# Optimization experiments

Measured on AMD Instinct MI355X. Metric: run time of the kernel, lower is better.

## Reference

```python
import jax, jax.numpy as jnp
import numpy as np

HEADS = 16
THETA = 10000.0


def _rope(x, pos):
    # x: [b, h, s, d_k], pos: [b, s] int
    d_k = x.shape[-1]
    inv_freq = 1.0 / (THETA ** (jnp.arange(0, d_k, 2, dtype=jnp.float32) / d_k))  # [d_k/2]
    ang = pos[..., None].astype(jnp.float32) * inv_freq                           # [b, s, d_k/2]
    cos = jnp.cos(ang)[:, None, :, :]  # [b, 1, s, d_k/2] broadcast over heads
    sin = jnp.sin(ang)[:, None, :, :]
    x_even = x[..., 0::2]
    x_odd = x[..., 1::2]
    r_even = x_even * cos - x_odd * sin
    r_odd = x_even * sin + x_odd * cos
    return jnp.stack([r_even, r_odd], axis=-1).reshape(x.shape)


def setup_inputs() -> dict:
    key = jax.random.key(0)
    ks = jax.random.split(key, 5)
    B, S, D = 4, 2048, 1024
    std = float(np.sqrt(1.0 / D))
    def w(k):
        return jnp.clip(jax.random.normal(k, (D, D), jnp.float32) * std, -3 * std, 3 * std)
    return {
        "x": jax.random.normal(ks[0], (B, S, D), jnp.float32),
        "token_positions": jnp.broadcast_to(jnp.arange(S, dtype=jnp.int32), (B, S)),
        "wq": w(ks[1]),
        "wk": w(ks[2]),
        "wv": w(ks[3]),
        "wo": w(ks[4]),
    }


def reference(x, token_positions, wq, wk, wv, wo):
    B, S, D = x.shape
    h = HEADS
    dk = D // h
    # Projections: einsum 'hd d, ... s d -> ... s hd' == x @ W.T
    def proj(w):
        return jnp.einsum('bsd,kd->bsk', x, w).reshape(B, S, h, dk).transpose(0, 2, 1, 3)
    q = _rope(proj(wq), token_positions)  # [b,h,s,dk]
    k = _rope(proj(wk), token_positions)
    v = proj(wv)
    scores = jnp.einsum('bhqd,bhkd->bhqk', q, k) / np.sqrt(dk).astype(np.float32)
    causal = jnp.tril(jnp.ones((S, S), bool))
    scores = jnp.where(causal, scores, jnp.finfo(scores.dtype).min)
    attn = jax.nn.softmax(scores, axis=-1)
    out = jnp.einsum('bhqk,bhkd->bhqd', attn, v)        # [b,h,s,dk]
    out = out.transpose(0, 2, 1, 3).reshape(B, S, D)    # [b,s,h*dk]
    return jnp.einsum('bsv,dv->bsd', out, wo)
```

## Files before the change

### kernel.cpp

```cpp
#include <hip/hip_runtime.h>
#include <hip/hip_bf16.h>
#include <stdint.h>

typedef __bf16 bf16;
typedef __bf16 bf16x4 __attribute__((ext_vector_type(4)));
typedef __bf16 bf16x8 __attribute__((ext_vector_type(8)));
typedef float f32x4 __attribute__((ext_vector_type(4)));
typedef float f32x16 __attribute__((ext_vector_type(16)));

#define GLDS16(g, l) __builtin_amdgcn_global_load_lds( \
    (const __attribute__((address_space(1))) void*)(g), \
    (__attribute__((address_space(3))) void*)(l), 16, 0, 0)

static constexpr int S = 2048;

__global__ __launch_bounds__(256) void cvt_all(const float* __restrict__ x,
                                               const float* __restrict__ wq,
                                               const float* __restrict__ wk,
                                               const float* __restrict__ wv,
                                               const float* __restrict__ wo,
                                               const int* __restrict__ tp,
                                               bf16* __restrict__ xb,
                                               bf16* __restrict__ wqkvb,
                                               bf16* __restrict__ wob,
                                               bf16* __restrict__ tabc,
                                               bf16* __restrict__ tabs) {
  const int bid = blockIdx.x;
  if (bid >= 6144) {
    int idx = (bid - 6144) * 256 + threadIdx.x;
    int row = idx >> 5, pp = idx & 31;
    float p = (float)tp[row];
    float ang = p * exp2f((float)pp * -0.4152410118609203f);
    float sn, cs;
    sincosf(ang, &sn, &cs);
    tabc[idx] = (bf16)cs;
    tabs[idx] = (bf16)sn;
    return;
  }
  const float* src;
  bf16* dst;
  int i;
  if (bid < 4096) {
    src = x; dst = xb; i = bid * 256 + threadIdx.x;
  } else {
    int w = (bid - 4096) >> 9;
    i = ((bid - 4096) & 511) * 256 + threadIdx.x;
    src = (w == 0) ? wq : (w == 1) ? wk : (w == 2) ? wv : wo;
    dst = (w == 3) ? wob : wqkvb + (size_t)w * 1048576;
  }
  const float4* p = (const float4*)src + (size_t)i * 2;
  float4 a = p[0], b = p[1];
  bf16x8 o;
  o[0] = (bf16)a.x; o[1] = (bf16)a.y; o[2] = (bf16)a.z; o[3] = (bf16)a.w;
  o[4] = (bf16)b.x; o[5] = (bf16)b.y; o[6] = (bf16)b.z; o[7] = (bf16)b.w;
  *((bf16x8*)dst + i) = o;
}

template <int MODE>
__global__ __launch_bounds__(256, 3) void gemm_k(const bf16* __restrict__ xA,
                                                 const bf16* __restrict__ wB,
                                                 const bf16* __restrict__ tabc,
                                                 const bf16* __restrict__ tabs,
                                                 bf16* __restrict__ oq,
                                                 bf16* __restrict__ ok,
                                                 bf16* __restrict__ ov,
                                                 float* __restrict__ outf) {
  constexpr int K = 1024;
  __shared__ __align__(16) char lds[49152];
  const int t = threadIdx.x, l = t & 63, wid = t >> 6;
  const int wm = wid >> 1, wn = wid & 1;
  const int bm = blockIdx.x, bn = blockIdx.y;

  int sel, tA, tB;
  const bf16 *Ap, *Bp;
  if (MODE == 0) {
    if (bn < 16) {
      sel = bn >> 3;
      tA = bm;
      tB = bn & 7;
      Ap = xA + (size_t)tA * 128 * K;
      Bp = wB + (size_t)(sel * 1024 + tB * 128) * K;
    } else {
      sel = 2;
      tA = bn - 16;
      tB = bm;
      Ap = wB + (size_t)(2048 + tA * 128) * K;
      Bp = xA + (size_t)tB * 128 * K;
    }
  } else {
    sel = 3;
    tA = bm; tB = bn;
    Ap = xA + (size_t)tA * 128 * K;
    Bp = wB + (size_t)tB * 128 * K;
  }

  const int lrow = l >> 2;
  const int csrc = ((l & 3) ^ ((l >> 3) & 3)) * 8;
  const bf16* aS = Ap + (size_t)(wid * 32 + lrow) * K + csrc;
  const bf16* bS = Bp + (size_t)(wid * 32 + lrow) * K + csrc;

  auto stage = [&](int kt, char* base) {
    GLDS16(aS + kt, base + (wid * 32) * 64);
    GLDS16(aS + (size_t)16 * K + kt, base + (wid * 32 + 16) * 64);
    GLDS16(bS + kt, base + 8192 + (wid * 32) * 64);
    GLDS16(bS + (size_t)16 * K + kt, base + 8192 + (wid * 32 + 16) * 64);
  };

  int offA[4], offB[4];
#pragma unroll
  for (int f = 0; f < 4; f++) {
    int ra = wm * 64 + f * 16 + (l & 15);
    offA[f] = ra * 64 + (((l >> 4) ^ ((ra >> 1) & 3)) * 16);
    int rb = wn * 64 + f * 16 + (l & 15);
    offB[f] = 8192 + rb * 64 + (((l >> 4) ^ ((rb >> 1) & 3)) * 16);
  }

  f32x4 acc[4][4] = {};

  char* cur = lds;
  char* nxt = lds + 16384;
  char* ovr = lds + 32768;
  stage(0, cur);
  stage(32, nxt);
#pragma unroll 1
  for (int t_ = 0; t_ < 32; ++t_) {
    if (t_ + 2 < 32) {
      stage((t_ + 2) * 32, ovr);
      asm volatile("s_waitcnt vmcnt(8)" ::: "memory");
    } else if (t_ + 1 < 32) {
      asm volatile("s_waitcnt vmcnt(4)" ::: "memory");
    } else {
      asm volatile("s_waitcnt vmcnt(0)" ::: "memory");
    }
    __builtin_amdgcn_s_barrier();
    __builtin_amdgcn_sched_barrier(0);

    bf16x8 af[4], bg[4];
#pragma unroll
    for (int f = 0; f < 4; f++) {
      af[f] = *(const bf16x8*)(cur + offA[f]);
      bg[f] = *(const bf16x8*)(cur + offB[f]);
    }
    __builtin_amdgcn_s_setprio(1);
#pragma unroll
    for (int mi = 0; mi < 4; mi++)
#pragma unroll
      for (int ni = 0; ni < 4; ni++)
        acc[mi][ni] = __builtin_amdgcn_mfma_f32_16x16x32_bf16(
            af[mi], bg[ni], acc[mi][ni], 0, 0, 0);
    __builtin_amdgcn_s_setprio(0);
    asm volatile("s_waitcnt lgkmcnt(0)" ::: "memory");
    __builtin_amdgcn_sched_barrier(0);
    __builtin_amdgcn_s_barrier();
    char* tmp = cur; cur = nxt; nxt = ovr; ovr = tmp;
  }

  if (MODE == 2) {
    const int rbase = tA * 128 + wm * 64 + (l >> 4) * 4;
    const int cbase = tB * 128 + wn * 64 + (l & 15);
#pragma unroll
    for (int mi = 0; mi < 4; mi++)
#pragma unroll
      for (int ni = 0; ni < 4; ni++)
#pragma unroll
        for (int r = 0; r < 4; r++)
          outf[(size_t)(rbase + mi * 16 + r) * 1024 + cbase + ni * 16] =
              acc[mi][ni][r];
    return;
  }

#pragma unroll
  for (int mi = 0; mi < 4; mi++)
#pragma unroll
    for (int ni = 0; ni < 4; ni++)
#pragma unroll
      for (int r = 0; r < 4; r++) {
        int row = wm * 64 + mi * 16 + (l >> 4) * 4 + r;
        int col = wn * 64 + ni * 16 + (l & 15);
        *(bf16*)(lds + row * 272 + col * 2) = (bf16)acc[mi][ni][r];
      }
  __syncthreads();

#pragma unroll 2
  for (int i = 0; i < 8; ++i) {
    const int id = t + 256 * i;
    const int row = id >> 4, ch = id & 15;
    bf16x8 v8 = *(const bf16x8*)(lds + row * 272 + ch * 16);
    if (sel < 2) {
      const int m = tA * 128 + row;
      const int g = ch & 7;
      bf16x4 tc = *(const bf16x4*)(tabc + m * 32 + g * 4);
      bf16x4 tsn = *(const bf16x4*)(tabs + m * 32 + g * 4);
      bf16x8 o;
#pragma unroll
      for (int j = 0; j < 4; j++) {
        float cs = (float)tc[j], sn = (float)tsn[j];
        float e = (float)v8[2 * j], od = (float)v8[2 * j + 1];
        o[2 * j]     = (bf16)(e * cs - od * sn);
        o[2 * j + 1] = (bf16)(e * sn + od * cs);
      }
      bf16* dst = (sel == 0) ? oq : ok;
      const int h = tB * 2 + (ch >> 3);
      size_t idx = ((size_t)((m >> 11) * 16 + h) << 17) +
                   ((size_t)(m & 2047) << 6) + g * 8;
      *(bf16x8*)(dst + idx) = o;
    } else {
      const int dd = tA * 128 + row;
      const int h = dd >> 6;
      const int s0 = tB * 128 + ch * 8;
      size_t idx = ((size_t)((s0 >> 11) * 16 + h) << 17) +
                   ((size_t)(dd & 63) << 11) + (s0 & 2047);
      *(bf16x8*)(ov + idx) = v8;
    }
  }
}

__global__ __launch_bounds__(512, 4) void attn_k(const bf16* __restrict__ q,
                                                 const bf16* __restrict__ k,
                                                 const bf16* __restrict__ vt,
                                                 bf16* __restrict__ att) {
  __shared__ bf16 Ks[3][4096];
  __shared__ bf16 Vs[3][4096];

  const int t = threadIdx.x, l = t & 63, w = t >> 6;
  const int hi2 = l >> 5, q5 = l & 31;

  const int raw = blockIdx.x;
  const int r2 = raw & 255;
  const int wg = (r2 & 7) * 32 + (r2 >> 3);
  const int bh = ((raw < 256) ? 0 : 32) + (wg >> 3);
  const int qt = (raw < 256) ? (wg & 7) : 7 - (wg & 7);

  const bf16* qb = q + (size_t)bh * S * 64;
  const bf16* kb = k + (size_t)bh * S * 64;
  const bf16* vb = vt + (size_t)bh * 64 * S;

  const int lrow = l >> 3;
  const int clog = ((l & 7) ^ (lrow & 7)) * 8;

  auto stage = [&](int nt, int b) {
    GLDS16(kb + (size_t)(nt * 64 + w * 8 + lrow) * 64 + clog, &Ks[b][w * 512]);
    GLDS16(vb + (size_t)(w * 8 + lrow) * S + nt * 64 + clog, &Vs[b][w * 512]);
  };

  const int swz = (q5 & 7) << 4;
  int kaddr[4], vaddr[8];
#pragma unroll
  for (int c = 0; c < 4; c++)
    kaddr[c] = q5 * 128 + ((32 * c + 16 * hi2) ^ swz);
#pragma unroll
  for (int m = 0; m < 8; m++)
    vaddr[m] = q5 * 128 + ((16 * m) ^ swz) + 8 * hi2;

  const int b_ = bh >> 4, h_ = bh & 15;
  const char* KsB = (const char*)&Ks[0][0];
  const char* VsB = (const char*)&Vs[0][0];

  const int wqbase = qt * 256 + w * 32;
  const int qrow = wqbase + q5;
  bf16x8 qf[4];
#pragma unroll
  for (int c = 0; c < 4; c++) {
    bf16x8 rq = *(const bf16x8*)&qb[(size_t)qrow * 64 + 16 * c + 8 * hi2];
    bf16x8 s_;
#pragma unroll
    for (int j2 = 0; j2 < 8; j2++)
      s_[j2] = (bf16)((float)rq[j2] * 0.18033688011112042f);
    qf[c] = s_;
  }

  f32x16 acc[2] = {};
  float l_r = 0.f;
  const int nkv = 4 * qt + 4;
  const int qmaxw = wqbase + 31;

  int cur = 0, nxt = 1, ovr = 2;
  stage(0, 0);
  stage(1, 1);
#pragma unroll 1
  for (int nt = 0; nt < nkv; ++nt) {
    if (nt + 2 < nkv) {
      stage(nt + 2, ovr);
      asm volatile("s_waitcnt vmcnt(4)" ::: "memory");
    } else if (nt + 1 < nkv) {
      asm volatile("s_waitcnt vmcnt(2)" ::: "memory");
    } else {
      asm volatile("s_waitcnt vmcnt(0)" ::: "memory");
    }
    __builtin_amdgcn_s_barrier();
    __builtin_amdgcn_sched_barrier(0);

    const bool live = (64 * nt) <= qmaxw;
    if (live) {
      const int bo = cur * 8192;
      float rs = 0.f;
#pragma unroll
      for (int T = 0; T < 2; T++) {
        f32x16 sc = {};
        __builtin_amdgcn_s_setprio(1);
#pragma unroll
        for (int c = 0; c < 4; c++) {
          bf16x8 kf = *(const bf16x8*)(KsB + bo + T * 4096 + kaddr[c]);
          sc = __builtin_amdgcn_mfma_f32_32x32x16_bf16(kf, qf[c], sc, 0, 0, 0);
        }
        __builtin_amdgcn_s_setprio(0);

        if (64 * nt + 32 * T + 31 > wqbase) {
#pragma unroll
          for (int r = 0; r < 16; r++) {
            int kvg = 64 * nt + 32 * T + (r & 3) + 8 * (r >> 2) + 4 * hi2;
            if (kvg > qrow) sc[r] = -1e30f;
          }
        }

        bf16x8 pa0, pa1;
#pragma unroll
        for (int r = 0; r < 8; r++) {
          float p0 = __builtin_amdgcn_exp2f(sc[r]);
          float p1 = __builtin_amdgcn_exp2f(sc[8 + r]);
          rs += p0 + p1;
          pa0[r] = (bf16)p0;
          pa1[r] = (bf16)p1;
        }

        __builtin_amdgcn_s_setprio(1);
#pragma unroll
        for (int dt = 0; dt < 2; dt++) {
          bf16x4 v0 = *(const bf16x4*)(VsB + bo + dt * 4096 + vaddr[4 * T]);
          bf16x4 v1 = *(const bf16x4*)(VsB + bo + dt * 4096 + vaddr[4 * T + 1]);
          bf16x8 bv;
#pragma unroll
          for (int j2 = 0; j2 < 4; j2++) { bv[j2] = v0[j2]; bv[4 + j2] = v1[j2]; }
          acc[dt] = __builtin_amdgcn_mfma_f32_32x32x16_bf16(pa0, bv, acc[dt], 0, 0, 0);
          v0 = *(const bf16x4*)(VsB + bo + dt * 4096 + vaddr[4 * T + 2]);
          v1 = *(const bf16x4*)(VsB + bo + dt * 4096 + vaddr[4 * T + 3]);
#pragma unroll
          for (int j2 = 0; j2 < 4; j2++) { bv[j2] = v0[j2]; bv[4 + j2] = v1[j2]; }
          acc[dt] = __builtin_amdgcn_mfma_f32_32x32x16_bf16(pa1, bv, acc[dt], 0, 0, 0);
        }
        __builtin_amdgcn_s_setprio(0);
      }
      rs += __shfl_xor(rs, 32);
      l_r += rs;
    }

    asm volatile("s_waitcnt lgkmcnt(0)" ::: "memory");
    __builtin_amdgcn_sched_barrier(0);
    __builtin_amdgcn_s_barrier();
    int t3 = cur; cur = nxt; nxt = ovr; ovr = t3;
  }

  float linv = 1.f / l_r;
#pragma unroll
  for (int r = 0; r < 16; r++) {
    int rmap = (r & 3) + 8 * (r >> 2) + 4 * hi2;
    float li = __shfl(linv, rmap);
    int rowq = wqbase + rmap;
    size_t rb = ((size_t)(b_ * S + rowq) << 10) + h_ * 64 + q5;
#pragma unroll
    for (int dt = 0; dt < 2; dt++)
      att[rb + 32 * dt] = (bf16)(acc[dt][r] * li);
  }
}

extern "C" void kernel_launch(void* const* d_in, const int* in_sizes, int n_in,
                              void* d_out, int out_size, void* d_ws, size_t ws_size,
                              hipStream_t stream) {
  const float* x  = (const float*)d_in[0];
  const int* tp   = (const int*)d_in[1];
  const float* wq = (const float*)d_in[2];
  const float* wk = (const float*)d_in[3];
  const float* wv = (const float*)d_in[4];
  const float* wo = (const float*)d_in[5];
  float* out = (float*)d_out;

  char* ws = (char*)d_ws;
  const size_t TEN = 16777216;
  bf16* x_bf    = (bf16*)(ws);
  bf16* q_bf    = (bf16*)(ws + TEN);
  bf16* k_bf    = (bf16*)(ws + 2 * TEN);
  bf16* v_bf    = (bf16*)(ws + 3 * TEN);
  bf16* wqkv_bf = (bf16*)(ws + 4 * TEN);
  bf16* wo_bf   = wqkv_bf + 3 * 1048576;
  bf16* tabc    = wo_bf + 1048576;
  bf16* tabs    = tabc + 262144;
  bf16* att_bf  = x_bf;

  cvt_all<<<7168, 256, 0, stream>>>(x, wq, wk, wv, wo, tp, x_bf, wqkv_bf,
                                    wo_bf, tabc, tabs);

  dim3 gq(64, 24);
  gemm_k<0><<<gq, 256, 0, stream>>>(x_bf, wqkv_bf, tabc, tabs, q_bf, k_bf,
                                    v_bf, nullptr);

  attn_k<<<512, 512, 0, stream>>>(q_bf, k_bf, v_bf, att_bf);

  dim3 go(64, 8);
  gemm_k<2><<<go, 256, 0, stream>>>(att_bf, wo_bf, nullptr, nullptr, nullptr,
                                    nullptr, nullptr, out);
}
```

Before: 154.4 us.

## Use 32x32x16 MFMA with two-wave 128-thread GEMM blocks

Reworks the projection and output GEMM kernel to run 2 waves per 128x128 tile instead of 4. Each wave now computes a 128x64 subtile with 32x32x16 bf16 MFMAs in place of 16x16x32. Global-to-LDS staging, the LDS swizzle, the wait counts and the epilogue index mapping are all rewritten to match. The aim is fewer LDS fragment reads per MFMA and higher per-wave arithmetic intensity, at the cost of more accumulator registers per wave and fewer waves to hide latency.

```diff
diff --git a/kernel.cpp b/kernel.cpp
--- a/kernel.cpp
+++ b/kernel.cpp
@@ -57,7 +57,7 @@
 }
 
 template <int MODE>
-__global__ __launch_bounds__(256, 3) void gemm_k(const bf16* __restrict__ xA,
+__global__ __launch_bounds__(128, 2) void gemm_k(const bf16* __restrict__ xA,
                                                  const bf16* __restrict__ wB,
                                                  const bf16* __restrict__ tabc,
                                                  const bf16* __restrict__ tabs,
@@ -67,9 +67,9 @@
                                                  float* __restrict__ outf) {
   constexpr int K = 1024;
   __shared__ __align__(16) char lds[49152];
-  const int t = threadIdx.x, l = t & 63, wid = t >> 6;
-  const int wm = wid >> 1, wn = wid & 1;
+  const int t = threadIdx.x, l = t & 63, w = t >> 6;
   const int bm = blockIdx.x, bn = blockIdx.y;
+  const int l5 = l & 31, hi = l >> 5;
 
   int sel, tA, tB;
   const bf16 *Ap, *Bp;
@@ -95,27 +95,41 @@
   }
 
   const int lrow = l >> 2;
-  const int csrc = ((l & 3) ^ ((l >> 3) & 3)) * 8;
-  const bf16* aS = Ap + (size_t)(wid * 32 + lrow) * K + csrc;
-  const bf16* bS = Bp + (size_t)(wid * 32 + lrow) * K + csrc;
+  const int swe = (((l >> 3) & 3) ^ ((l >> 5) & 1));
+  const int cs_e = ((l & 3) ^ swe) * 8;
+  const int cs_o = ((l & 3) ^ swe ^ 2) * 8;
+  const bf16* aS = Ap + (size_t)(w * 64 + lrow) * K;
+  const bf16* bS = Bp + (size_t)(w * 64 + lrow) * K;
 
   auto stage = [&](int kt, char* base) {
-    GLDS16(aS + kt, base + (wid * 32) * 64);
-    GLDS16(aS + (size_t)16 * K + kt, base + (wid * 32 + 16) * 64);
-    GLDS16(bS + kt, base + 8192 + (wid * 32) * 64);
-    GLDS16(bS + (size_t)16 * K + kt, base + 8192 + (wid * 32 + 16) * 64);
+#pragma unroll
+    for (int g = 0; g < 4; g++) {
+      const int cs = (g & 1) ? cs_o : cs_e;
+      GLDS16(aS + (size_t)(g * 16) * K + kt + cs, base + (w * 64 + g * 16) * 64);
+      GLDS16(bS + (size_t)(g * 16) * K + kt + cs,
+             base + 8192 + (w * 64 + g * 16) * 64);
+    }
   };
 
-  int offA[4], offB[4];
-#pragma unroll
-  for (int f = 0; f < 4; f++) {
-    int ra = wm * 64 + f * 16 + (l & 15);
-    offA[f] = ra * 64 + (((l >> 4) ^ ((ra >> 1) & 3)) * 16);
-    int rb = wn * 64 + f * 16 + (l & 15);
-    offB[f] = 8192 + rb * 64 + (((l >> 4) ^ ((rb >> 1) & 3)) * 16);
-  }
-
-  f32x4 acc[4][4] = {};
+  int offA[4][2], offB[2][2];
+#pragma unroll
+  for (int mi = 0; mi < 4; mi++)
+#pragma unroll
+    for (int kc = 0; kc < 2; kc++) {
+      int ra = mi * 32 + l5;
+      int swr = ((ra >> 1) ^ (ra >> 3)) & 3;
+      offA[mi][kc] = ra * 64 + (((2 * kc + hi) ^ swr) * 16);
+    }
+#pragma unroll
+  for (int ni = 0; ni < 2; ni++)
+#pragma unroll
+    for (int kc = 0; kc < 2; kc++) {
+      int rb = w * 64 + ni * 32 + l5;
+      int swr = ((rb >> 1) ^ (rb >> 3)) & 3;
+      offB[ni][kc] = 8192 + rb * 64 + (((2 * kc + hi) ^ swr) * 16);
+    }
+
+  f32x16 acc[4][2] = {};
 
   char* cur = lds;
   char* nxt = lds + 16384;
@@ -126,28 +140,36 @@
   for (int t_ = 0; t_ < 32; ++t_) {
     if (t_ + 2 < 32) {
       stage((t_ + 2) * 32, ovr);
+      asm volatile("s_waitcnt vmcnt(16)" ::: "memory");
+    } else if (t_ + 1 < 32) {
       asm volatile("s_waitcnt vmcnt(8)" ::: "memory");
-    } else if (t_ + 1 < 32) {
-      asm volatile("s_waitcnt vmcnt(4)" ::: "memory");
     } else {
       asm volatile("s_waitcnt vmcnt(0)" ::: "memory");
     }
     __builtin_amdgcn_s_barrier();
     __builtin_amdgcn_sched_barrier(0);
 
-    bf16x8 af[4], bg[4];
-#pragma unroll
-    for (int f = 0; f < 4; f++) {
-      af[f] = *(const bf16x8*)(cur + offA[f]);
-      bg[f] = *(const bf16x8*)(cur + offB[f]);
-    }
+    bf16x8 af[4][2], bg[2][2];
+#pragma unroll
+    for (int mi = 0; mi < 4; mi++)
+#pragma unroll
+      for (int kc = 0; kc < 2; kc++)
+        af[mi][kc] = *(const bf16x8*)(cur + offA[mi][kc]);
+#pragma unroll
+    for (int ni = 0; ni < 2; ni++)
+#pragma unroll
+      for (int kc = 0; kc < 2; kc++)
+        bg[ni][kc] = *(const bf16x8*)(cur + offB[ni][kc]);
+
     __builtin_amdgcn_s_setprio(1);
 #pragma unroll
     for (int mi = 0; mi < 4; mi++)
 #pragma unroll
-      for (int ni = 0; ni < 4; ni++)
-        acc[mi][ni] = __builtin_amdgcn_mfma_f32_16x16x32_bf16(
-            af[mi], bg[ni], acc[mi][ni], 0, 0, 0);
+      for (int ni = 0; ni < 2; ni++)
+#pragma unroll
+        for (int kc = 0; kc < 2; kc++)
+          acc[mi][ni] = __builtin_amdgcn_mfma_f32_32x32x16_bf16(
+              af[mi][kc], bg[ni][kc], acc[mi][ni], 0, 0, 0);
     __builtin_amdgcn_s_setprio(0);
     asm volatile("s_waitcnt lgkmcnt(0)" ::: "memory");
     __builtin_amdgcn_sched_barrier(0);
@@ -156,34 +178,34 @@
   }
 
   if (MODE == 2) {
-    const int rbase = tA * 128 + wm * 64 + (l >> 4) * 4;
-    const int cbase = tB * 128 + wn * 64 + (l & 15);
 #pragma unroll
     for (int mi = 0; mi < 4; mi++)
 #pragma unroll
-      for (int ni = 0; ni < 4; ni++)
-#pragma unroll
-        for (int r = 0; r < 4; r++)
-          outf[(size_t)(rbase + mi * 16 + r) * 1024 + cbase + ni * 16] =
-              acc[mi][ni][r];
+      for (int ni = 0; ni < 2; ni++)
+#pragma unroll
+        for (int r = 0; r < 16; r++) {
+          int gm = tA * 128 + mi * 32 + (r & 3) + 8 * (r >> 2) + 4 * hi;
+          int gn = tB * 128 + w * 64 + ni * 32 + l5;
+          outf[(size_t)gm * 1024 + gn] = acc[mi][ni][r];
+        }
     return;
   }
 
 #pragma unroll
   for (int mi = 0; mi < 4; mi++)
 #pragma unroll
-    for (int ni = 0; ni < 4; ni++)
-#pragma unroll
-      for (int r = 0; r < 4; r++) {
-        int row = wm * 64 + mi * 16 + (l >> 4) * 4 + r;
-        int col = wn * 64 + ni * 16 + (l & 15);
+    for (int ni = 0; ni < 2; ni++)
+#pragma unroll
+      for (int r = 0; r < 16; r++) {
+        int row = mi * 32 + (r & 3) + 8 * (r >> 2) + 4 * hi;
+        int col = w * 64 + ni * 32 + l5;
         *(bf16*)(lds + row * 272 + col * 2) = (bf16)acc[mi][ni][r];
       }
   __syncthreads();
 
 #pragma unroll 2
-  for (int i = 0; i < 8; ++i) {
-    const int id = t + 256 * i;
+  for (int i = 0; i < 16; ++i) {
+    const int id = t + 128 * i;
     const int row = id >> 4, ch = id & 15;
     bf16x8 v8 = *(const bf16x8*)(lds + row * 272 + ch * 16);
     if (sel < 2) {
@@ -390,12 +412,12 @@
                                     wo_bf, tabc, tabs);
 
   dim3 gq(64, 24);
-  gemm_k<0><<<gq, 256, 0, stream>>>(x_bf, wqkv_bf, tabc, tabs, q_bf, k_bf,
+  gemm_k<0><<<gq, 128, 0, stream>>>(x_bf, wqkv_bf, tabc, tabs, q_bf, k_bf,
                                     v_bf, nullptr);
 
   attn_k<<<512, 512, 0, stream>>>(q_bf, k_bf, v_bf, att_bf);
 
   dim3 go(64, 8);
-  gemm_k<2><<<go, 256, 0, stream>>>(att_bf, wo_bf, nullptr, nullptr, nullptr,
+  gemm_k<2><<<go, 128, 0, stream>>>(att_bf, wo_bf, nullptr, nullptr, nullptr,
                                     nullptr, nullptr, out);
 }
```

Measured after the change: 173.7 us. 1.13x slower.

## Replace QKV projection GEMM with 256x256-tile 8-wave pipelined kernel

Applied to the files above, without the earlier changes.

The fused QKV projection moves from a 128x128, 4-wave, triple-buffered GEMM to a 256x256-tile, 8-wave kernel with 128KB of LDS, double buffering over K=64 slices and four interleaved compute quadrants. Half-tile global-to-LDS loads are staggered between the MFMA phases. The larger tile is meant to raise arithmetic intensity and cut redundant global reads of x and the weights. The RoPE/transposed-V epilogue is now done in two LDS passes. In exchange, occupancy drops to one or two blocks per CU and only 384 blocks are launched, so wave quantization and barrier overhead could offset the gain.

```diff
diff --git a/kernel.cpp b/kernel.cpp
--- a/kernel.cpp
+++ b/kernel.cpp
@@ -56,43 +56,222 @@
   *((bf16x8*)dst + i) = o;
 }
 
-template <int MODE>
-__global__ __launch_bounds__(256, 3) void gemm_k(const bf16* __restrict__ xA,
+__global__ __launch_bounds__(512, 2) void gemm8p(const bf16* __restrict__ xA,
                                                  const bf16* __restrict__ wB,
                                                  const bf16* __restrict__ tabc,
                                                  const bf16* __restrict__ tabs,
                                                  bf16* __restrict__ oq,
                                                  bf16* __restrict__ ok,
-                                                 bf16* __restrict__ ov,
-                                                 float* __restrict__ outf) {
+                                                 bf16* __restrict__ ov) {
+  constexpr int K = 1024;
+  __shared__ __align__(16) char lds[131072];
+  const int t = threadIdx.x, l = t & 63, w = t >> 6;
+  const int wm = w >> 2, wn = w & 3;
+  const int bm = blockIdx.x, bn = blockIdx.y;
+
+  int sel;
+  const bf16 *Ap, *Bp;
+  if (bn < 8) {
+    sel = bn >> 2;
+    Ap = xA + (size_t)bm * 256 * K;
+    Bp = wB + (size_t)bn * 256 * K;
+  } else {
+    sel = 2;
+    Ap = wB + (size_t)bn * 256 * K;
+    Bp = xA + (size_t)bm * 256 * K;
+  }
+
+  const int lr8 = l >> 3;
+  const int clog = ((l & 7) ^ (lr8 & 7)) * 8;
+  const int rsA0 = wm * 128 + (wn * 2 + 0) * 8;
+  const int rsA1 = wm * 128 + (wn * 2 + 1) * 8;
+  const int c0B0 = (w >> 1) * 64 + ((w & 1) * 2 + 0) * 8;
+  const int c0B1 = (w >> 1) * 64 + ((w & 1) * 2 + 1) * 8;
+
+  auto stA = [&](int T, int rs) {
+    GLDS16(Ap + (size_t)(rs + lr8) * K + T * 64 + clog,
+           lds + (T & 1) * 65536 + rs * 128);
+  };
+  auto stB = [&](int T, int c0) {
+    GLDS16(Bp + (size_t)(c0 + lr8) * K + T * 64 + clog,
+           lds + (T & 1) * 65536 + 32768 + c0 * 128);
+  };
+
+  const int sw0 = (((l >> 4)) ^ (l & 7)) * 16;
+  const int sw1 = ((4 + (l >> 4)) ^ (l & 7)) * 16;
+  const int rowA = wm * 128 + (l & 15);
+  const int colB = wn * 64 + (l & 15);
+  const int baseA0 = rowA * 128 + sw0, baseA1 = rowA * 128 + sw1;
+  const int baseB0 = 32768 + colB * 128 + sw0, baseB1 = 32768 + colB * 128 + sw1;
+
+  f32x4 acc[8][4] = {};
+
+  stA(0, rsA0); stA(0, rsA1);
+  stB(0, 32 + c0B0); stB(0, 32 + c0B1);
+  stA(0, 64 + rsA0); stA(0, 64 + rsA1);
+  stB(0, c0B0); stB(0, c0B1);
+  stA(1, rsA0); stA(1, rsA1);
+  stB(1, 32 + c0B0); stB(1, 32 + c0B1);
+  asm volatile("s_waitcnt vmcnt(4)" ::: "memory");
+  __builtin_amdgcn_s_barrier();
+
+#pragma unroll 1
+  for (int T = 0; T < 16; ++T) {
+    const char* bb = lds + (T & 1) * 65536;
+    bf16x8 a0[4][2], a1[4][2], b0[2][2], b1[2][2];
+
+#pragma unroll
+    for (int mi = 0; mi < 4; mi++) {
+      a0[mi][0] = *(const bf16x8*)(bb + baseA0 + mi * 2048);
+      a0[mi][1] = *(const bf16x8*)(bb + baseA1 + mi * 2048);
+    }
+#pragma unroll
+    for (int ni = 0; ni < 2; ni++) {
+      b0[ni][0] = *(const bf16x8*)(bb + baseB0 + ni * 2048);
+      b0[ni][1] = *(const bf16x8*)(bb + baseB1 + ni * 2048);
+    }
+    if (T + 1 < 16) { stA(T + 1, 64 + rsA0); stA(T + 1, 64 + rsA1); }
+    __builtin_amdgcn_s_barrier();
+    asm volatile("s_waitcnt lgkmcnt(0)" ::: "memory");
+    __builtin_amdgcn_sched_barrier(0);
+    __builtin_amdgcn_s_setprio(1);
+#pragma unroll
+    for (int mi = 0; mi < 4; mi++)
+#pragma unroll
+      for (int ni = 0; ni < 2; ni++)
+#pragma unroll
+        for (int ks = 0; ks < 2; ks++)
+          acc[mi][ni] = __builtin_amdgcn_mfma_f32_16x16x32_bf16(
+              a0[mi][ks], b0[ni][ks], acc[mi][ni], 0, 0, 0);
+    __builtin_amdgcn_s_setprio(0);
+    __builtin_amdgcn_s_barrier();
+
+#pragma unroll
+    for (int ni = 0; ni < 2; ni++) {
+      b1[ni][0] = *(const bf16x8*)(bb + baseB0 + (2 + ni) * 2048);
+      b1[ni][1] = *(const bf16x8*)(bb + baseB1 + (2 + ni) * 2048);
+    }
+    if (T + 1 < 16) { stB(T + 1, c0B0); stB(T + 1, c0B1); }
+    __builtin_amdgcn_s_barrier();
+    asm volatile("s_waitcnt lgkmcnt(0)" ::: "memory");
+    __builtin_amdgcn_sched_barrier(0);
+    __builtin_amdgcn_s_setprio(1);
+#pragma unroll
+    for (int mi = 0; mi < 4; mi++)
+#pragma unroll
+      for (int ni = 0; ni < 2; ni++)
+#pragma unroll
+        for (int ks = 0; ks < 2; ks++)
+          acc[mi][2 + ni] = __builtin_amdgcn_mfma_f32_16x16x32_bf16(
+              a0[mi][ks], b1[ni][ks], acc[mi][2 + ni], 0, 0, 0);
+    __builtin_amdgcn_s_setprio(0);
+    __builtin_amdgcn_s_barrier();
+
+#pragma unroll
+    for (int mi = 0; mi < 4; mi++) {
+      a1[mi][0] = *(const bf16x8*)(bb + baseA0 + (4 + mi) * 2048);
+      a1[mi][1] = *(const bf16x8*)(bb + baseA1 + (4 + mi) * 2048);
+    }
+    if (T + 2 < 16) { stA(T + 2, rsA0); stA(T + 2, rsA1); }
+    __builtin_amdgcn_s_barrier();
+    asm volatile("s_waitcnt lgkmcnt(0)" ::: "memory");
+    __builtin_amdgcn_sched_barrier(0);
+    __builtin_amdgcn_s_setprio(1);
+#pragma unroll
+    for (int mi = 0; mi < 4; mi++)
+#pragma unroll
+      for (int ni = 0; ni < 2; ni++)
+#pragma unroll
+        for (int ks = 0; ks < 2; ks++)
+          acc[4 + mi][2 + ni] = __builtin_amdgcn_mfma_f32_16x16x32_bf16(
+              a1[mi][ks], b1[ni][ks], acc[4 + mi][2 + ni], 0, 0, 0);
+    __builtin_amdgcn_s_setprio(0);
+    __builtin_amdgcn_s_barrier();
+
+    if (T + 2 < 16) { stB(T + 2, 32 + c0B0); stB(T + 2, 32 + c0B1); }
+    __builtin_amdgcn_s_setprio(1);
+#pragma unroll
+    for (int mi = 0; mi < 4; mi++)
+#pragma unroll
+      for (int ni = 0; ni < 2; ni++)
+#pragma unroll
+        for (int ks = 0; ks < 2; ks++)
+          acc[4 + mi][ni] = __builtin_amdgcn_mfma_f32_16x16x32_bf16(
+              a1[mi][ks], b0[ni][ks], acc[4 + mi][ni], 0, 0, 0);
+    __builtin_amdgcn_s_setprio(0);
+    if (T < 14) {
+      asm volatile("s_waitcnt vmcnt(4)" ::: "memory");
+    } else {
+      asm volatile("s_waitcnt vmcnt(0)" ::: "memory");
+    }
+    __builtin_amdgcn_s_barrier();
+  }
+
+  __syncthreads();
+
+#pragma unroll 1
+  for (int pass = 0; pass < 2; ++pass) {
+    if (wm == pass) {
+#pragma unroll
+      for (int mi = 0; mi < 8; mi++)
+#pragma unroll
+        for (int ni = 0; ni < 4; ni++)
+#pragma unroll
+          for (int r = 0; r < 4; r++) {
+            int row = mi * 16 + (l >> 4) * 4 + r;
+            int col = wn * 64 + ni * 16 + (l & 15);
+            *(bf16*)(lds + row * 528 + col * 2) = (bf16)acc[mi][ni][r];
+          }
+    }
+    __syncthreads();
+#pragma unroll 2
+    for (int i = 0; i < 8; ++i) {
+      int id = t + 512 * i;
+      int rloc = id >> 5, ch = id & 31;
+      int row = pass * 128 + rloc;
+      bf16x8 v8 = *(const bf16x8*)(lds + rloc * 528 + ch * 16);
+      if (sel < 2) {
+        const int m = bm * 256 + row;
+        const int g = ch & 7;
+        bf16x4 tc = *(const bf16x4*)(tabc + m * 32 + g * 4);
+        bf16x4 tsn = *(const bf16x4*)(tabs + m * 32 + g * 4);
+        bf16x8 o;
+#pragma unroll
+        for (int j = 0; j < 4; j++) {
+          float cs = (float)tc[j], sn = (float)tsn[j];
+          float e = (float)v8[2 * j], od = (float)v8[2 * j + 1];
+          o[2 * j]     = (bf16)(e * cs - od * sn);
+          o[2 * j + 1] = (bf16)(e * sn + od * cs);
+        }
+        bf16* dst = (sel == 0) ? oq : ok;
+        const int h = (bn & 3) * 4 + (ch >> 3);
+        size_t idx = ((size_t)((m >> 11) * 16 + h) << 17) +
+                     ((size_t)(m & 2047) << 6) + g * 8;
+        *(bf16x8*)(dst + idx) = o;
+      } else {
+        const int dd = (bn - 8) * 256 + row;
+        const int h = dd >> 6;
+        const int s0 = bm * 256 + ch * 8;
+        size_t idx = ((size_t)((s0 >> 11) * 16 + h) << 17) +
+                     ((size_t)(dd & 63) << 11) + (s0 & 2047);
+        *(bf16x8*)(ov + idx) = v8;
+      }
+    }
+    __syncthreads();
+  }
+}
+
+__global__ __launch_bounds__(256, 3) void gemm_wo(const bf16* __restrict__ xA,
+                                                  const bf16* __restrict__ wB,
+                                                  float* __restrict__ outf) {
   constexpr int K = 1024;
   __shared__ __align__(16) char lds[49152];
   const int t = threadIdx.x, l = t & 63, wid = t >> 6;
   const int wm = wid >> 1, wn = wid & 1;
   const int bm = blockIdx.x, bn = blockIdx.y;
 
-  int sel, tA, tB;
-  const bf16 *Ap, *Bp;
-  if (MODE == 0) {
-    if (bn < 16) {
-      sel = bn >> 3;
-      tA = bm;
-      tB = bn & 7;
-      Ap = xA + (size_t)tA * 128 * K;
-      Bp = wB + (size_t)(sel * 1024 + tB * 128) * K;
-    } else {
-      sel = 2;
-      tA = bn - 16;
-      tB = bm;
-      Ap = wB + (size_t)(2048 + tA * 128) * K;
-      Bp = xA + (size_t)tB * 128 * K;
-    }
-  } else {
-    sel = 3;
-    tA = bm; tB = bn;
-    Ap = xA + (size_t)tA * 128 * K;
-    Bp = wB + (size_t)tB * 128 * K;
-  }
+  const bf16* Ap = xA + (size_t)bm * 128 * K;
+  const bf16* Bp = wB + (size_t)bn * 128 * K;
 
   const int lrow = l >> 2;
   const int csrc = ((l & 3) ^ ((l >> 3) & 3)) * 8;
@@ -155,64 +334,16 @@
     char* tmp = cur; cur = nxt; nxt = ovr; ovr = tmp;
   }
 
-  if (MODE == 2) {
-    const int rbase = tA * 128 + wm * 64 + (l >> 4) * 4;
-    const int cbase = tB * 128 + wn * 64 + (l & 15);
-#pragma unroll
-    for (int mi = 0; mi < 4; mi++)
-#pragma unroll
-      for (int ni = 0; ni < 4; ni++)
-#pragma unroll
-        for (int r = 0; r < 4; r++)
-          outf[(size_t)(rbase + mi * 16 + r) * 1024 + cbase + ni * 16] =
-              acc[mi][ni][r];
-    return;
-  }
-
+  const int rbase = bm * 128 + wm * 64 + (l >> 4) * 4;
+  const int cbase = bn * 128 + wn * 64 + (l & 15);
 #pragma unroll
   for (int mi = 0; mi < 4; mi++)
 #pragma unroll
     for (int ni = 0; ni < 4; ni++)
 #pragma unroll
-      for (int r = 0; r < 4; r++) {
-        int row = wm * 64 + mi * 16 + (l >> 4) * 4 + r;
-        int col = wn * 64 + ni * 16 + (l & 15);
-        *(bf16*)(lds + row * 272 + col * 2) = (bf16)acc[mi][ni][r];
-      }
-  __syncthreads();
-
-#pragma unroll 2
-  for (int i = 0; i < 8; ++i) {
-    const int id = t + 256 * i;
-    const int row = id >> 4, ch = id & 15;
-    bf16x8 v8 = *(const bf16x8*)(lds + row * 272 + ch * 16);
-    if (sel < 2) {
-      const int m = tA * 128 + row;
-      const int g = ch & 7;
-      bf16x4 tc = *(const bf16x4*)(tabc + m * 32 + g * 4);
-      bf16x4 tsn = *(const bf16x4*)(tabs + m * 32 + g * 4);
-      bf16x8 o;
-#pragma unroll
-      for (int j = 0; j < 4; j++) {
-        float cs = (float)tc[j], sn = (float)tsn[j];
-        float e = (float)v8[2 * j], od = (float)v8[2 * j + 1];
-        o[2 * j]     = (bf16)(e * cs - od * sn);
-        o[2 * j + 1] = (bf16)(e * sn + od * cs);
-      }
-      bf16* dst = (sel == 0) ? oq : ok;
-      const int h = tB * 2 + (ch >> 3);
-      size_t idx = ((size_t)((m >> 11) * 16 + h) << 17) +
-                   ((size_t)(m & 2047) << 6) + g * 8;
-      *(bf16x8*)(dst + idx) = o;
-    } else {
-      const int dd = tA * 128 + row;
-      const int h = dd >> 6;
-      const int s0 = tB * 128 + ch * 8;
-      size_t idx = ((size_t)((s0 >> 11) * 16 + h) << 17) +
-                   ((size_t)(dd & 63) << 11) + (s0 & 2047);
-      *(bf16x8*)(ov + idx) = v8;
-    }
-  }
+      for (int r = 0; r < 4; r++)
+        outf[(size_t)(rbase + mi * 16 + r) * 1024 + cbase + ni * 16] =
+            acc[mi][ni][r];
 }
 
 __global__ __launch_bounds__(512, 4) void attn_k(const bf16* __restrict__ q,
@@ -389,13 +520,11 @@
   cvt_all<<<7168, 256, 0, stream>>>(x, wq, wk, wv, wo, tp, x_bf, wqkv_bf,
                                     wo_bf, tabc, tabs);
 
-  dim3 gq(64, 24);
-  gemm_k<0><<<gq, 256, 0, stream>>>(x_bf, wqkv_bf, tabc, tabs, q_bf, k_bf,
-                                    v_bf, nullptr);
+  dim3 gq(32, 12);
+  gemm8p<<<gq, 512, 0, stream>>>(x_bf, wqkv_bf, tabc, tabs, q_bf, k_bf, v_bf);
 
   attn_k<<<512, 512, 0, stream>>>(q_bf, k_bf, v_bf, att_bf);
 
   dim3 go(64, 8);
-  gemm_k<2><<<go, 256, 0, stream>>>(att_bf, wo_bf, nullptr, nullptr, nullptr,
-                                    nullptr, nullptr, out);
+  gemm_wo<<<go, 256, 0, stream>>>(att_bf, wo_bf, out);
 }
```

New measurement: 161.9 us. 4.8% more time.

## Double-buffer 128-row KV stages in attention instead of triple-buffering 64-row tiles

Applied to the files above, without the earlier changes.

The attention kernel's K/V staging moves from three 64-row LDS buffers to two 128-row buffers. Each barrier-delimited stage now processes two KV subtiles, which halves the barriers and the row-sum shuffles per KV row. The cost is a prefetch distance of one stage instead of two, and shared memory per block grows from 48KB to 64KB, which may reduce how many blocks fit on a CU.

```diff
diff --git a/kernel.cpp b/kernel.cpp
--- a/kernel.cpp
+++ b/kernel.cpp
@@ -219,8 +219,8 @@
                                                  const bf16* __restrict__ k,
                                                  const bf16* __restrict__ vt,
                                                  bf16* __restrict__ att) {
-  __shared__ bf16 Ks[3][4096];
-  __shared__ bf16 Vs[3][4096];
+  __shared__ bf16 Ks[2][8192];
+  __shared__ bf16 Vs[2][8192];
 
   const int t = threadIdx.x, l = t & 63, w = t >> 6;
   const int hi2 = l >> 5, q5 = l & 31;
@@ -238,9 +238,15 @@
   const int lrow = l >> 3;
   const int clog = ((l & 7) ^ (lrow & 7)) * 8;
 
-  auto stage = [&](int nt, int b) {
-    GLDS16(kb + (size_t)(nt * 64 + w * 8 + lrow) * 64 + clog, &Ks[b][w * 512]);
-    GLDS16(vb + (size_t)(w * 8 + lrow) * S + nt * 64 + clog, &Vs[b][w * 512]);
+  auto stage = [&](int st, int b) {
+#pragma unroll
+    for (int sub = 0; sub < 2; sub++) {
+      const int nt = 2 * st + sub;
+      GLDS16(kb + (size_t)(nt * 64 + w * 8 + lrow) * 64 + clog,
+             &Ks[b][sub * 4096 + w * 512]);
+      GLDS16(vb + (size_t)(w * 8 + lrow) * S + nt * 64 + clog,
+             &Vs[b][sub * 4096 + w * 512]);
+    }
   };
 
   const int swz = (q5 & 7) << 4;
@@ -271,29 +277,28 @@
 
   f32x16 acc[2] = {};
   float l_r = 0.f;
-  const int nkv = 4 * qt + 4;
+  const int nst = 2 * qt + 2;
   const int qmaxw = wqbase + 31;
 
-  int cur = 0, nxt = 1, ovr = 2;
   stage(0, 0);
-  stage(1, 1);
 #pragma unroll 1
-  for (int nt = 0; nt < nkv; ++nt) {
-    if (nt + 2 < nkv) {
-      stage(nt + 2, ovr);
+  for (int s = 0; s < nst; ++s) {
+    if (s + 1 < nst) {
+      stage(s + 1, (s + 1) & 1);
       asm volatile("s_waitcnt vmcnt(4)" ::: "memory");
-    } else if (nt + 1 < nkv) {
-      asm volatile("s_waitcnt vmcnt(2)" ::: "memory");
     } else {
       asm volatile("s_waitcnt vmcnt(0)" ::: "memory");
     }
     __builtin_amdgcn_s_barrier();
     __builtin_amdgcn_sched_barrier(0);
 
-    const bool live = (64 * nt) <= qmaxw;
-    if (live) {
-      const int bo = cur * 8192;
-      float rs = 0.f;
+    const int bo_buf = (s & 1) * 16384;
+    float rs = 0.f;
+#pragma unroll
+    for (int sub = 0; sub < 2; sub++) {
+      const int nt = 2 * s + sub;
+      if (64 * nt > qmaxw) continue;
+      const int bo = bo_buf + sub * 8192;
 #pragma unroll
       for (int T = 0; T < 2; T++) {
         f32x16 sc = {};
@@ -340,14 +345,13 @@
         }
         __builtin_amdgcn_s_setprio(0);
       }
-      rs += __shfl_xor(rs, 32);
-      l_r += rs;
-    }
+    }
+    rs += __shfl_xor(rs, 32);
+    l_r += rs;
 
     asm volatile("s_waitcnt lgkmcnt(0)" ::: "memory");
     __builtin_amdgcn_sched_barrier(0);
     __builtin_amdgcn_s_barrier();
-    int t3 = cur; cur = nxt; nxt = ovr; ovr = t3;
   }
 
   float linv = 1.f / l_r;
```

Measured after the change: 148.5 us. -3.8%, faster.
